# Performance work log

Hardware: AMD Instinct MI355X
Metric: run time of the kernel (lower is better)

## Reference

```python
import jax, jax.numpy as jnp
import numpy as np
import math

EMB = 100

def setup_inputs() -> dict:
    key = jax.random.key(0)
    ks = jax.random.split(key, 10)
    B, L = 4, 512
    src = jax.random.normal(ks[0], (B, L, EMB), dtype=jnp.float32)
    att_w = jnp.ones((3,), dtype=jnp.float32)
    conv_w1 = jax.random.normal(ks[1], (10, 1, 1, EMB), dtype=jnp.float32) * 0.05
    conv_b1 = jax.random.normal(ks[2], (10,), dtype=jnp.float32) * 0.05
    conv_w2 = jax.random.normal(ks[3], (10, 1, 2, EMB), dtype=jnp.float32) * 0.05
    conv_b2 = jax.random.normal(ks[4], (10,), dtype=jnp.float32) * 0.05
    conv_w3 = jax.random.normal(ks[5], (10, 1, 3, EMB), dtype=jnp.float32) * 0.05
    conv_b3 = jax.random.normal(ks[6], (10,), dtype=jnp.float32) * 0.05
    lin_w = jax.random.normal(ks[7], (30, 2), dtype=jnp.float32) * 0.05
    lin_b = jax.random.normal(ks[8], (2,), dtype=jnp.float32) * 0.05
    return {"src": src, "att_w": att_w,
            "conv_w1": conv_w1, "conv_b1": conv_b1,
            "conv_w2": conv_w2, "conv_b2": conv_b2,
            "conv_w3": conv_w3, "conv_b3": conv_b3,
            "lin_w": lin_w, "lin_b": lin_b}

def _dot_attention(x):
    # [B,L,L] scores, softmax over keys, weighted sum
    scores = jnp.einsum('bqd,bkd->bqk', x, x)
    return jnp.einsum('bqk,bkd->bqd', jax.nn.softmax(scores, axis=-1), x)

def _scaled_dot_attention(q, k, v):
    d_k = k.shape[-1]
    scores = jnp.einsum('bqd,bkd->bqk', q, k) / math.sqrt(d_k)
    return jnp.einsum('bqk,bkd->bqd', jax.nn.softmax(scores, axis=-1), v)

def _additive_attention(q, k, v):
    # explicit O(L^2 * d) broadcast as in the original module
    scores = jnp.tanh(q[:, :, None, :] + k[:, None, :, :]).sum(axis=-1)  # [B,L,L]
    return jnp.einsum('bqk,bkd->bqd', jax.nn.softmax(scores, axis=-1), v)

def _conv_branch(x, w, b, ws):
    # x: [B,1,L,EMB], w: [10,1,ws,EMB]; torch padding=(ws-1, 0) pads both sides in H
    y = jax.lax.conv_general_dilated(
        x, w, window_strides=(1, 1),
        padding=[(ws - 1, ws - 1), (0, 0)],
        dimension_numbers=('NCHW', 'OIHW', 'NCHW'))
    y = jax.nn.relu(y + b[None, :, None, None])  # [B,10,L+ws-1,1]
    return jnp.max(y[..., 0], axis=2)            # global max-pool over time -> [B,10]

def reference(src, att_w, conv_w1, conv_b1, conv_w2, conv_b2, conv_w3, conv_b3, lin_w, lin_b):
    a1 = _dot_attention(src)
    a2 = _additive_attention(src, src, src)
    a3 = _scaled_dot_attention(src, src, src)
    w = att_w / att_w.sum()
    attn = w[0] * a1 + w[1] * a2 + w[2] * a3
    x = (src + attn)[:, None, :, :]  # [B,1,L,EMB]
    pooled = jnp.concatenate([
        _conv_branch(x, conv_w1, conv_b1, 1),
        _conv_branch(x, conv_w2, conv_b2, 2),
        _conv_branch(x, conv_w3, conv_b3, 3),
    ], axis=1)  # [B,30]; dropout is identity in eval mode
    return pooled @ lin_w + lin_b
```

## Files before the change

kernel.cpp:

```cpp
#include <hip/hip_runtime.h>

#define B_ 4
#define L_ 512
#define D_ 100

__device__ __forceinline__ float fexp2(float x) { return __builtin_amdgcn_exp2f(x); }
__device__ __forceinline__ float frcp(float x)  { return __builtin_amdgcn_rcpf(x); }

__global__ __launch_bounds__(256) void k1_scores(const float* __restrict__ x,
                                                 float* __restrict__ S,
                                                 float* __restrict__ T,
                                                 float* __restrict__ Zp,
                                                 int* __restrict__ counter,
                                                 float* __restrict__ pooled) {
  __shared__ float2 XQ[32 * 102];
  __shared__ float2 XK[32 * 102];
  const int tid = threadIdx.x;
  const int job = blockIdx.x;
  if (job == 0) {
    if (tid < B_ * 30) pooled[tid] = 0.0f;
    if (tid == 128) *counter = 0;
  }
  int b, qt, kt;
  if (job < 480) {
    b = job / 120;
    int r = job - b * 120;
    qt = 0;
    while (r >= 15 - qt) { r -= 15 - qt; ++qt; }
    kt = qt + 1 + r;
  } else {
    int dj = job - 480;
    b = dj >> 4;
    qt = kt = dj & 15;
  }
  const bool diag = (kt == qt);
  const float C = 2.8853900817779268f;
  const float L2E = 1.4426950408889634f;
  const float* xb = x + (size_t)b * L_ * D_;
  for (int i = tid; i < 32 * D_; i += 256) {
    int r = i / D_, c = i - r * D_;
    float xq = xb[(qt * 32 + r) * D_ + c];
    XQ[r * 102 + c] = make_float2(xq, fexp2(xq * C));
    if (!diag) {
      float xk = xb[(kt * 32 + r) * D_ + c];
      XK[r * 102 + c] = make_float2(xk, fexp2(xk * C));
    }
  }
  __syncthreads();
  const float2* XKp = diag ? XQ : XK;
  const int tx = tid & 15, ty = tid >> 4;
  float s00 = 0, s01 = 0, s10 = 0, s11 = 0;
  float r00 = 0, r01 = 0, r10 = 0, r11 = 0;
  const float2* qp0 = &XQ[ty * 102];
  const float2* qp1 = &XQ[(ty + 16) * 102];
  const float2* kp0 = &XKp[tx * 102];
  const float2* kp1 = &XKp[(tx + 16) * 102];
#pragma unroll 2
  for (int d = 0; d < D_; d += 2) {
    float4 A0 = *(const float4*)&qp0[d];
    float4 A1 = *(const float4*)&qp1[d];
    float4 B0 = *(const float4*)&kp0[d];
    float4 B1 = *(const float4*)&kp1[d];
    s00 += A0.x * B0.x + A0.z * B0.z;
    s01 += A0.x * B1.x + A0.z * B1.z;
    s10 += A1.x * B0.x + A1.z * B0.z;
    s11 += A1.x * B1.x + A1.z * B1.z;
    r00 += frcp(fmaf(A0.y, B0.y, 1.0f)) + frcp(fmaf(A0.w, B0.w, 1.0f));
    r01 += frcp(fmaf(A0.y, B1.y, 1.0f)) + frcp(fmaf(A0.w, B1.w, 1.0f));
    r10 += frcp(fmaf(A1.y, B0.y, 1.0f)) + frcp(fmaf(A1.w, B0.w, 1.0f));
    r11 += frcp(fmaf(A1.y, B1.y, 1.0f)) + frcp(fmaf(A1.w, B1.w, 1.0f));
  }
  float t00 = (float)D_ - 2.0f * r00;
  float t01 = (float)D_ - 2.0f * r01;
  float t10 = (float)D_ - 2.0f * r10;
  float t11 = (float)D_ - 2.0f * r11;
  float e1_00 = fexp2(fmaf(s00, L2E, -120.0f)), e1_01 = fexp2(fmaf(s01, L2E, -120.0f));
  float e1_10 = fexp2(fmaf(s10, L2E, -120.0f)), e1_11 = fexp2(fmaf(s11, L2E, -120.0f));
  float e2_00 = fexp2(fmaf(t00, L2E, -32.0f)),  e2_01 = fexp2(fmaf(t01, L2E, -32.0f));
  float e2_10 = fexp2(fmaf(t10, L2E, -32.0f)),  e2_11 = fexp2(fmaf(t11, L2E, -32.0f));
  const float L2E10 = 0.14426950408889634f;
  float e3_00 = fexp2(s00 * L2E10), e3_01 = fexp2(s01 * L2E10);
  float e3_10 = fexp2(s10 * L2E10), e3_11 = fexp2(s11 * L2E10);

  const int q0r = qt * 32 + ty, q1r = q0r + 16;
  const int k0 = kt * 32 + tx, k1 = k0 + 16;
  float* Sb = S + (size_t)b * L_ * L_;
  float* Tb = T + (size_t)b * L_ * L_;
  Sb[q0r * L_ + k0] = s00; Sb[q0r * L_ + k1] = s01;
  Sb[q1r * L_ + k0] = s10; Sb[q1r * L_ + k1] = s11;
  Tb[q0r * L_ + k0] = t00; Tb[q0r * L_ + k1] = t01;
  Tb[q1r * L_ + k0] = t10; Tb[q1r * L_ + k1] = t11;

  float rs[3][2];
  rs[0][0] = e1_00 + e1_01; rs[0][1] = e1_10 + e1_11;
  rs[1][0] = e2_00 + e2_01; rs[1][1] = e2_10 + e2_11;
  rs[2][0] = e3_00 + e3_01; rs[2][1] = e3_10 + e3_11;
#pragma unroll
  for (int o = 8; o > 0; o >>= 1) {
#pragma unroll
    for (int e = 0; e < 3; ++e) {
      rs[e][0] += __shfl_xor(rs[e][0], o);
      rs[e][1] += __shfl_xor(rs[e][1], o);
    }
  }
  if (tx == 0) {
#pragma unroll
    for (int e = 0; e < 3; ++e) {
      Zp[(((size_t)b * L_ + q0r) * 16 + kt) * 3 + e] = rs[e][0];
      Zp[(((size_t)b * L_ + q1r) * 16 + kt) * 3 + e] = rs[e][1];
    }
  }

  if (diag) return;

  float cs_[3][2];
  cs_[0][0] = e1_00 + e1_10; cs_[0][1] = e1_01 + e1_11;
  cs_[1][0] = e2_00 + e2_10; cs_[1][1] = e2_01 + e2_11;
  cs_[2][0] = e3_00 + e3_10; cs_[2][1] = e3_01 + e3_11;
#pragma unroll
  for (int o = 16; o <= 32; o <<= 1) {
#pragma unroll
    for (int e = 0; e < 3; ++e) {
      cs_[e][0] += __shfl_xor(cs_[e][0], o);
      cs_[e][1] += __shfl_xor(cs_[e][1], o);
    }
  }
  __syncthreads();
  float* xkf = (float*)XK;
  float* M = xkf;
  float* colred = xkf + 1104;
  const int wv = tid >> 6, lane = tid & 63;
  if ((lane >> 4) == 0) {
#pragma unroll
    for (int e = 0; e < 3; ++e) {
      colred[wv * 96 + tx * 6 + e * 2 + 0] = cs_[e][0];
      colred[wv * 96 + tx * 6 + e * 2 + 1] = cs_[e][1];
    }
  }
  __syncthreads();
  if (tid < 96) {
    int txx = tid / 6, j = tid - txx * 6;
    float v = colred[0 * 96 + txx * 6 + j] + colred[1 * 96 + txx * 6 + j] +
              colred[2 * 96 + txx * 6 + j] + colred[3 * 96 + txx * 6 + j];
    int e = j >> 1, half = j & 1;
    int krow = kt * 32 + txx + half * 16;
    Zp[(((size_t)b * L_ + krow) * 16 + qt) * 3 + e] = v;
  }
  const int mo = ty * 33 + tx;
  M[mo] = s00; M[mo + 16] = s01;
  M[mo + 16 * 33] = s10; M[mo + 16 * 33 + 16] = s11;
  __syncthreads();
#pragma unroll
  for (int j = 0; j < 4; ++j) {
    int idx = tid + 256 * j, kr = idx >> 5, qc = idx & 31;
    Sb[(kt * 32 + kr) * L_ + qt * 32 + qc] = M[qc * 33 + kr];
  }
  __syncthreads();
  M[mo] = t00; M[mo + 16] = t01;
  M[mo + 16 * 33] = t10; M[mo + 16 * 33 + 16] = t11;
  __syncthreads();
#pragma unroll
  for (int j = 0; j < 4; ++j) {
    int idx = tid + 256 * j, kr = idx >> 5, qc = idx & 31;
    Tb[(kt * 32 + kr) * L_ + qt * 32 + qc] = M[qc * 33 + kr];
  }
}

__global__ __launch_bounds__(256) void k2_fused(const float* __restrict__ x,
    const float* __restrict__ S, const float* __restrict__ T,
    const float* __restrict__ Zp, const float* __restrict__ attw,
    const float* __restrict__ w1, const float* __restrict__ b1,
    const float* __restrict__ w2, const float* __restrict__ b2,
    const float* __restrict__ w3, const float* __restrict__ b3,
    const float* __restrict__ lw, const float* __restrict__ lb,
    float* __restrict__ pooled, int* __restrict__ counter,
    float* __restrict__ out) {
  __shared__ float wl[30 * 304];
  __shared__ float cc[6][3];
  __shared__ float P[6][512];
  __shared__ float R[2][6][128];
  __shared__ float X2L[6][104];
  __shared__ int lastFlag;
  const int tid = threadIdx.x;
  const int b = blockIdx.x >> 7, q0 = (blockIdx.x & 127) * 4;
  const float L2E = 1.4426950408889634f, L2E10 = 0.14426950408889634f;

  for (int i = tid; i < 30 * 300; i += 256) {
    int c = i / 300, rest = i - c * 300;
    int h = rest / D_, dd = rest - h * D_;
    int ws = 1 + c / 10;
    int hh = h - (3 - ws);
    float wv = 0.0f;
    if (hh >= 0) {
      if (ws == 1)      wv = w1[c * D_ + dd];
      else if (ws == 2) wv = w2[(c - 10) * 2 * D_ + hh * D_ + dd];
      else              wv = w3[(c - 20) * 3 * D_ + hh * D_ + dd];
    }
    wl[c * 304 + h * D_ + dd] = wv;
  }
  if (tid < 18) {
    int row = tid / 3, j = tid - row * 3;
    int qr = q0 + row;
    float cv = 0.0f;
    if (qr < L_) {
      const float* zp = Zp + ((size_t)b * L_ + qr) * 16 * 3 + j;
      float z = 0.0f;
#pragma unroll
      for (int t = 0; t < 16; ++t) z += zp[t * 3];
      float winv = frcp(attw[0] + attw[1] + attw[2]);
      cv = attw[j] * winv * frcp(z);
    }
    cc[row][j] = cv;
  }
  __syncthreads();

  for (int i = tid; i < 6 * 512; i += 256) {
    int row = i >> 9, kk = i & 511;
    int qr = q0 + row;
    float pv = 0.0f;
    if (qr < L_) {
      size_t o = ((size_t)b * L_ + qr) * (size_t)L_ + kk;
      float s = S[o], t = T[o];
      pv = cc[row][0] * fexp2(fmaf(s, L2E, -120.0f)) +
           cc[row][1] * fexp2(fmaf(t, L2E, -32.0f)) +
           cc[row][2] * fexp2(s * L2E10);
    }
    P[row][kk] = pv;
  }
  __syncthreads();

  const int d = tid & 127, kh = tid >> 7;
  float a0 = 0, a1 = 0, a2 = 0, a3 = 0, a4 = 0, a5 = 0;
  if (d < D_) {
    const float* xb = x + ((size_t)b * L_ + kh * 256) * D_;
    for (int g = 0; g < 64; ++g) {
      int kk = kh * 256 + g * 4;
      float x0 = xb[(g * 4 + 0) * D_ + d];
      float x1 = xb[(g * 4 + 1) * D_ + d];
      float x2 = xb[(g * 4 + 2) * D_ + d];
      float x3 = xb[(g * 4 + 3) * D_ + d];
      float4 p;
      p = *(const float4*)&P[0][kk]; a0 += p.x*x0 + p.y*x1 + p.z*x2 + p.w*x3;
      p = *(const float4*)&P[1][kk]; a1 += p.x*x0 + p.y*x1 + p.z*x2 + p.w*x3;
      p = *(const float4*)&P[2][kk]; a2 += p.x*x0 + p.y*x1 + p.z*x2 + p.w*x3;
      p = *(const float4*)&P[3][kk]; a3 += p.x*x0 + p.y*x1 + p.z*x2 + p.w*x3;
      p = *(const float4*)&P[4][kk]; a4 += p.x*x0 + p.y*x1 + p.z*x2 + p.w*x3;
      p = *(const float4*)&P[5][kk]; a5 += p.x*x0 + p.y*x1 + p.z*x2 + p.w*x3;
    }
  }
  R[kh][0][d] = a0; R[kh][1][d] = a1; R[kh][2][d] = a2;
  R[kh][3][d] = a3; R[kh][4][d] = a4; R[kh][5][d] = a5;
  __syncthreads();

  for (int i = tid; i < 6 * D_; i += 256) {
    int r = i / D_, dd = i - r * D_;
    int qr = q0 + r;
    float v = 0.0f;
    if (qr < L_)
      v = x[((size_t)b * L_ + qr) * D_ + dd] + R[0][r][dd] + R[1][r][dd];
    X2L[r][dd] = v;
  }
  __syncthreads();

  const int c = tid >> 3, tl = tid & 7;
  float vm = 0.0f;
  if (c < 30) {
    int t = -1;
    if (tl < 4) t = q0 + 2 + tl;
    else if (q0 == 0 && tl < 6) t = tl - 4;
    int wsz = 1 + c / 10;
    if (t >= 0 && t < L_ + wsz - 1) {
      float acc = 0.0f;
#pragma unroll
      for (int h = 0; h < 3; ++h) {
        int idx = t - 2 + h - q0;
        if (idx >= 0) {
          const float4* xr = (const float4*)&X2L[idx][0];
          const float4* wr = (const float4*)&wl[c * 304 + h * D_];
#pragma unroll 5
          for (int j = 0; j < 25; ++j) {
            float4 xv = xr[j], wv = wr[j];
            acc += xv.x * wv.x + xv.y * wv.y + xv.z * wv.z + xv.w * wv.w;
          }
        }
      }
      float bias = (wsz == 1) ? b1[c] : (wsz == 2 ? b2[c - 10] : b3[c - 20]);
      vm = fmaxf(acc + bias, 0.0f);
    }
  }
  vm = fmaxf(vm, __shfl_xor(vm, 1));
  vm = fmaxf(vm, __shfl_xor(vm, 2));
  vm = fmaxf(vm, __shfl_xor(vm, 4));
  if (c < 30 && tl == 0)
    atomicMax(reinterpret_cast<int*>(&pooled[b * 30 + c]), __float_as_int(vm));

  __syncthreads();
  if (tid == 0) {
    __threadfence();
    int old = atomicAdd(counter, 1);
    lastFlag = (old == 512 - 1);
  }
  __syncthreads();
  if (lastFlag && tid < B_ * 2) {
    int bb = tid >> 1, j = tid & 1;
    float acc = lb[j];
    int* pI = reinterpret_cast<int*>(pooled);
#pragma unroll
    for (int cch = 0; cch < 30; ++cch) {
      int pi = atomicMax(&pI[bb * 30 + cch], 0);
      acc = fmaf(__int_as_float(pi), lw[cch * 2 + j], acc);
    }
    out[bb * 2 + j] = acc;
  }
}

extern "C" void kernel_launch(void* const* d_in, const int* in_sizes, int n_in,
                              void* d_out, int out_size, void* d_ws, size_t ws_size,
                              hipStream_t stream) {
  const float* src  = (const float*)d_in[0];
  const float* attw = (const float*)d_in[1];
  const float* w1   = (const float*)d_in[2];
  const float* b1   = (const float*)d_in[3];
  const float* w2   = (const float*)d_in[4];
  const float* b2   = (const float*)d_in[5];
  const float* w3   = (const float*)d_in[6];
  const float* b3   = (const float*)d_in[7];
  const float* lw   = (const float*)d_in[8];
  const float* lb   = (const float*)d_in[9];

  float* S  = (float*)d_ws;
  float* T  = S + (size_t)B_ * L_ * L_;
  float* Zp = T + (size_t)B_ * L_ * L_;
  float* PL = Zp + (size_t)B_ * L_ * 16 * 3;
  int* counter = (int*)(PL + 128);
  float* out = (float*)d_out;

  hipLaunchKernelGGL(k1_scores, dim3(544), dim3(256), 0, stream,
                     src, S, T, Zp, counter, PL);
  hipLaunchKernelGGL(k2_fused, dim3(512), dim3(256), 0, stream,
                     src, S, T, Zp, attw, w1, b1, w2, b2, w3, b3, lw, lb,
                     PL, counter, out);
}
```

Measured before the change: 68.89 us.

## Restructure PV accumulation with float4 columns and k-split, redistribute conv dot products

The P·X accumulation in k2_fused now has each thread own four consecutive feature columns, loaded as float4, over a 64-key slice. Eight key slices are combined by a cross-half-wave shuffle and then a four-way shared-memory reduction, replacing the previous scalar-column, two-way key split. The conv stage now holds each channel's weights in registers and gives each of the 8 lanes a slice of the embedding for all 6 time positions, reducing with shuffles instead of one lane per time position looping over all 100 features. The intent is wider global loads, better use of each thread's data and more balanced conv work, at the cost of higher register pressure and extra reduction steps.

```diff
diff --git a/kernel.cpp b/kernel.cpp
--- a/kernel.cpp
+++ b/kernel.cpp
@@ -178,7 +178,7 @@
   __shared__ float wl[30 * 304];
   __shared__ float cc[6][3];
   __shared__ float P[6][512];
-  __shared__ float R[2][6][128];
+  __shared__ float R[4][6][104];
   __shared__ float X2L[6][104];
   __shared__ int lastFlag;
   const int tid = threadIdx.x;
@@ -229,27 +229,42 @@
   }
   __syncthreads();
 
-  const int d = tid & 127, kh = tid >> 7;
-  float a0 = 0, a1 = 0, a2 = 0, a3 = 0, a4 = 0, a5 = 0;
-  if (d < D_) {
-    const float* xb = x + ((size_t)b * L_ + kh * 256) * D_;
-    for (int g = 0; g < 64; ++g) {
-      int kk = kh * 256 + g * 4;
-      float x0 = xb[(g * 4 + 0) * D_ + d];
-      float x1 = xb[(g * 4 + 1) * D_ + d];
-      float x2 = xb[(g * 4 + 2) * D_ + d];
-      float x3 = xb[(g * 4 + 3) * D_ + d];
-      float4 p;
-      p = *(const float4*)&P[0][kk]; a0 += p.x*x0 + p.y*x1 + p.z*x2 + p.w*x3;
-      p = *(const float4*)&P[1][kk]; a1 += p.x*x0 + p.y*x1 + p.z*x2 + p.w*x3;
-      p = *(const float4*)&P[2][kk]; a2 += p.x*x0 + p.y*x1 + p.z*x2 + p.w*x3;
-      p = *(const float4*)&P[3][kk]; a3 += p.x*x0 + p.y*x1 + p.z*x2 + p.w*x3;
-      p = *(const float4*)&P[4][kk]; a4 += p.x*x0 + p.y*x1 + p.z*x2 + p.w*x3;
-      p = *(const float4*)&P[5][kk]; a5 += p.x*x0 + p.y*x1 + p.z*x2 + p.w*x3;
-    }
-  }
-  R[kh][0][d] = a0; R[kh][1][d] = a1; R[kh][2][d] = a2;
-  R[kh][3][d] = a3; R[kh][4][d] = a4; R[kh][5][d] = a5;
+  const int dq = tid & 31, ks = tid >> 5;
+  float4 acc[6];
+#pragma unroll
+  for (int r = 0; r < 6; ++r) acc[r] = make_float4(0.f, 0.f, 0.f, 0.f);
+  if (dq < 25) {
+    const float* xb = x + (size_t)b * L_ * D_;
+    const int kbase = ks * 64;
+    for (int g = 0; g < 16; ++g) {
+      int k = kbase + g * 4;
+      float4 xv0 = *(const float4*)&xb[(k + 0) * D_ + 4 * dq];
+      float4 xv1 = *(const float4*)&xb[(k + 1) * D_ + 4 * dq];
+      float4 xv2 = *(const float4*)&xb[(k + 2) * D_ + 4 * dq];
+      float4 xv3 = *(const float4*)&xb[(k + 3) * D_ + 4 * dq];
+#pragma unroll
+      for (int r = 0; r < 6; ++r) {
+        float4 p = *(const float4*)&P[r][k];
+        acc[r].x += p.x * xv0.x + p.y * xv1.x + p.z * xv2.x + p.w * xv3.x;
+        acc[r].y += p.x * xv0.y + p.y * xv1.y + p.z * xv2.y + p.w * xv3.y;
+        acc[r].z += p.x * xv0.z + p.y * xv1.z + p.z * xv2.z + p.w * xv3.z;
+        acc[r].w += p.x * xv0.w + p.y * xv1.w + p.z * xv2.w + p.w * xv3.w;
+      }
+    }
+  }
+#pragma unroll
+  for (int r = 0; r < 6; ++r) {
+    acc[r].x += __shfl_xor(acc[r].x, 32);
+    acc[r].y += __shfl_xor(acc[r].y, 32);
+    acc[r].z += __shfl_xor(acc[r].z, 32);
+    acc[r].w += __shfl_xor(acc[r].w, 32);
+  }
+  const int wv = tid >> 6;
+  if ((tid & 63) < 32 && dq < 25) {
+#pragma unroll
+    for (int r = 0; r < 6; ++r)
+      *(float4*)&R[wv][r][4 * dq] = acc[r];
+  }
   __syncthreads();
 
   for (int i = tid; i < 6 * D_; i += 256) {
@@ -257,42 +272,64 @@
     int qr = q0 + r;
     float v = 0.0f;
     if (qr < L_)
-      v = x[((size_t)b * L_ + qr) * D_ + dd] + R[0][r][dd] + R[1][r][dd];
+      v = x[((size_t)b * L_ + qr) * D_ + dd] +
+          R[0][r][dd] + R[1][r][dd] + R[2][r][dd] + R[3][r][dd];
     X2L[r][dd] = v;
   }
   __syncthreads();
 
-  const int c = tid >> 3, tl = tid & 7;
-  float vm = 0.0f;
-  if (c < 30) {
-    int t = -1;
-    if (tl < 4) t = q0 + 2 + tl;
-    else if (q0 == 0 && tl < 6) t = tl - 4;
-    int wsz = 1 + c / 10;
-    if (t >= 0 && t < L_ + wsz - 1) {
-      float acc = 0.0f;
+  const int c = tid >> 3, ds = tid & 7;
+  const int cS = (c < 30) ? c : 0;
+  const int wsz = 1 + cS / 10;
+  float4 wr[3][4];
+#pragma unroll
+  for (int h = 0; h < 3; ++h)
+#pragma unroll
+    for (int m = 0; m < 4; ++m) {
+      int j = ds + 8 * m;
+      wr[h][m] = (j < 25) ? *(const float4*)&wl[cS * 304 + h * D_ + 4 * j]
+                          : make_float4(0.f, 0.f, 0.f, 0.f);
+    }
+  float tacc[6];
+#pragma unroll
+  for (int tt = 0; tt < 6; ++tt) {
+    float a = 0.0f;
+    int t = (tt < 4) ? (q0 + 2 + tt) : ((q0 == 0) ? tt - 4 : -1);
+    if (t >= 0) {
 #pragma unroll
       for (int h = 0; h < 3; ++h) {
         int idx = t - 2 + h - q0;
         if (idx >= 0) {
-          const float4* xr = (const float4*)&X2L[idx][0];
-          const float4* wr = (const float4*)&wl[c * 304 + h * D_];
-#pragma unroll 5
-          for (int j = 0; j < 25; ++j) {
-            float4 xv = xr[j], wv = wr[j];
-            acc += xv.x * wv.x + xv.y * wv.y + xv.z * wv.z + xv.w * wv.w;
+#pragma unroll
+          for (int m = 0; m < 4; ++m) {
+            int j = ds + 8 * m;
+            if (j < 25) {
+              float4 xv = *(const float4*)&X2L[idx][4 * j];
+              float4 wv2 = wr[h][m];
+              a += xv.x * wv2.x + xv.y * wv2.y + xv.z * wv2.z + xv.w * wv2.w;
+            }
           }
         }
       }
-      float bias = (wsz == 1) ? b1[c] : (wsz == 2 ? b2[c - 10] : b3[c - 20]);
-      vm = fmaxf(acc + bias, 0.0f);
-    }
-  }
-  vm = fmaxf(vm, __shfl_xor(vm, 1));
-  vm = fmaxf(vm, __shfl_xor(vm, 2));
-  vm = fmaxf(vm, __shfl_xor(vm, 4));
-  if (c < 30 && tl == 0)
+    }
+    tacc[tt] = a;
+  }
+#pragma unroll
+  for (int tt = 0; tt < 6; ++tt) {
+    tacc[tt] += __shfl_xor(tacc[tt], 1);
+    tacc[tt] += __shfl_xor(tacc[tt], 2);
+    tacc[tt] += __shfl_xor(tacc[tt], 4);
+  }
+  if (c < 30 && ds == 0) {
+    float bias = (wsz == 1) ? b1[c] : (wsz == 2 ? b2[c - 10] : b3[c - 20]);
+    float vm = 0.0f;
+#pragma unroll
+    for (int tt = 0; tt < 6; ++tt) {
+      int t = (tt < 4) ? (q0 + 2 + tt) : ((q0 == 0) ? tt - 4 : -1);
+      if (t >= 0 && t < L_ + wsz - 1) vm = fmaxf(vm, fmaxf(tacc[tt] + bias, 0.0f));
+    }
     atomicMax(reinterpret_cast<int*>(&pooled[b * 30 + c]), __float_as_int(vm));
+  }
 
   __syncthreads();
   if (tid == 0) {
@@ -303,14 +340,14 @@
   __syncthreads();
   if (lastFlag && tid < B_ * 2) {
     int bb = tid >> 1, j = tid & 1;
-    float acc = lb[j];
+    float acc2 = lb[j];
     int* pI = reinterpret_cast<int*>(pooled);
 #pragma unroll
     for (int cch = 0; cch < 30; ++cch) {
       int pi = atomicMax(&pI[bb * 30 + cch], 0);
-      acc = fmaf(__int_as_float(pi), lw[cch * 2 + j], acc);
-    }
-    out[bb * 2 + j] = acc;
+      acc2 = fmaf(__int_as_float(pi), lw[cch * 2 + j], acc2);
+    }
+    out[bb * 2 + j] = acc2;
   }
 }
 
```

After: 62.71 us. 1.1x faster.
